# Kernel tuning notes

Hardware: AMD Instinct MI355X
Metric: run time of the kernel (lower is better)

The kernel has to match this reference:

```python
import jax, jax.numpy as jnp
import numpy as np

C = 64
HW = 21 * 21  # 441
NEIGHBOR_K = 3


def setup_inputs() -> dict:
    key = jax.random.key(0)
    k1, k2, k3, k4 = jax.random.split(key, 4)
    B1, B2 = 32, 25
    x1 = jax.random.normal(k1, (B1, C, 21, 21), dtype=jnp.float32)
    x2 = jax.random.normal(k2, (B2, C, 21, 21), dtype=jnp.float32)
    mask1 = jax.random.uniform(k3, (B1, 21, 21), dtype=jnp.float32)
    mask2 = jax.random.uniform(k4, (B2, 21, 21), dtype=jnp.float32)
    return {"x1": x1, "x2": x2, "mask1": mask1, "mask2": mask2}


def reference(x1, x2, mask1, mask2):
    B1 = x1.shape[0]
    B2 = x2.shape[0]
    q = x1.reshape(B1, C, HW)  # (B1, 64, 441) query descriptors
    s = x2.reshape(B2, C, HW)  # (B2, 64, 441) support descriptors
    # per-descriptor L2 norms over channel dim
    qn = jnp.linalg.norm(q, axis=1)  # (B1, 441)
    sn = jnp.linalg.norm(s, axis=1)  # (B2, 441)
    # cosine similarity between every query descriptor and every support descriptor
    inner = jnp.einsum('aci,bcj->abij', q, s)  # (B1, B2, 441, 441)
    sim = inner / (qn[:, None, :, None] * sn[None, :, None, :])
    # mask out invalid spatial positions on both sides
    sim = sim * mask1.reshape(B1, 1, HW, 1) * mask2.reshape(1, B2, 1, HW)
    # top-k nearest support descriptors per query descriptor, sum over all
    topk_vals, _ = jax.lax.top_k(sim, NEIGHBOR_K)  # (B1, B2, 441, k)
    return topk_vals.reshape(B1, B2, -1).sum(axis=2)  # (B1, B2)
```

## Files before the change

### kernel.cpp

```cpp
#include <hip/hip_runtime.h>
#include <math.h>

#define CCH 64
#define HW 441
#define HWP 448
#define NB2 25
#define PANEL (HWP * CCH)
#define TSTR 2048
#define NJT 14

typedef _Float16 half8 __attribute__((ext_vector_type(8)));
typedef __fp16 h2 __attribute__((ext_vector_type(2)));
typedef float f32x16 __attribute__((ext_vector_type(16)));

__global__ __launch_bounds__(64) void normalize_frag_kernel(
        const float* __restrict__ x1, const float* __restrict__ m1,
        const float* __restrict__ x2, const float* __restrict__ m2,
        _Float16* __restrict__ qh, _Float16* __restrict__ sh,
        float* __restrict__ out, int nout, int n1rows, int nrows) {
    int idx = blockIdx.x * blockDim.x + threadIdx.x;
    if (idx < nout) out[idx] = 0.f;
    if (idx >= nrows) return;
    const float* x; const float* mk; _Float16* outp; int rb;
    if (idx < n1rows) { x = x1; mk = m1; outp = qh; rb = idx; }
    else             { x = x2; mk = m2; outp = sh; rb = idx - n1rows; }
    int b = rb / HWP, i = rb - b * HWP;
    float vals[CCH];
    if (i < HW) {
        const float* xb = x + (size_t)b * CCH * HW + i;
        float ss = 0.f;
#pragma unroll
        for (int c = 0; c < CCH; ++c) { float v = xb[c * HW]; vals[c] = v; ss += v * v; }
        float scale = mk[b * HW + i] * rsqrtf(ss);
#pragma unroll
        for (int c = 0; c < CCH; ++c) vals[c] *= scale;
    } else {
#pragma unroll
        for (int c = 0; c < CCH; ++c) vals[c] = 0.f;
    }
    _Float16* pb = outp + (size_t)b * PANEL + (size_t)(i >> 5) * TSTR + (i & 31) * 8;
#pragma unroll
    for (int f = 0; f < 4; ++f) {
#pragma unroll
        for (int hh = 0; hh < 2; ++hh) {
            half8 h;
#pragma unroll
            for (int e = 0; e < 8; ++e) h[e] = (_Float16)vals[f * 16 + hh * 8 + e];
            *(half8*)(pb + f * 512 + hh * 256) = h;
        }
    }
}

static __device__ __forceinline__ h2 hmax2(h2 a, h2 b) {
    return __builtin_elementwise_max(a, b);
}
static __device__ __forceinline__ h2 hmin2(h2 a, h2 b) {
    return __builtin_elementwise_min(a, b);
}

#define PK_INSERT(v, p0, p1, p2)           \
    do {                                   \
        h2 _m = hmax2(p0, v);              \
        h2 _c = hmin2(p0, v);              \
        p0 = _m;                           \
        _m = hmax2(p1, _c);                \
        _c = hmin2(p1, _c);                \
        p1 = _m;                           \
        p2 = hmax2(p2, _c);                \
    } while (0)

#define MERGE3(t0, t1, t2, b0, b1, b2)            \
    do {                                          \
        float _m0 = fmaxf(t0, b0);                \
        float _n0 = fminf(t0, b0);                \
        float _m1 = fmaxf(t1, b1);                \
        float _t2 = fmaxf(t2, b2);                \
        t0 = _m0;                                 \
        t1 = fmaxf(_n0, _m1);                     \
        t2 = fmaxf(fminf(_n0, _m1), _t2);         \
    } while (0)

#define MFMA32(z, c, q) z = __builtin_amdgcn_mfma_f32_32x32x16_f16(c, q, z, 0, 0, 0)

__global__ __launch_bounds__(128, 5) void sim_topk_mfma(const _Float16* __restrict__ qh,
                                                        const _Float16* __restrict__ sh,
                                                        float* __restrict__ out) {
    int blk = blockIdx.x;
    int pair = blk / 7, g = blk - pair * 7;
    int a = pair / NB2, b = pair - a * NB2;
    int tid = threadIdx.x, wave = tid >> 6, lane = tid & 63;
    int hi = lane >> 5;
    const float NEG = -1e30f;
    const h2 NEGH = {(__fp16)-65504.f, (__fp16)-65504.f};

    const _Float16* qt = qh + (size_t)a * PANEL + (size_t)(g * 2 + wave) * TSTR + lane * 8;
    half8 qf0 = *(const half8*)(qt);
    half8 qf1 = *(const half8*)(qt + 512);
    half8 qf2 = *(const half8*)(qt + 1024);
    half8 qf3 = *(const half8*)(qt + 1536);

    const _Float16* sp = sh + (size_t)b * PANEL + lane * 8;
    half8 c0 = *(const half8*)(sp);
    half8 c1 = *(const half8*)(sp + 512);
    half8 c2 = *(const half8*)(sp + 1024);
    half8 c3 = *(const half8*)(sp + 1536);

    h2 p0 = NEGH, p1 = NEGH, p2 = NEGH;

    for (int jt = 0; jt < NJT - 1; ++jt) {
        const _Float16* np = sp + (size_t)(jt + 1) * TSTR;
        half8 n0 = *(const half8*)(np);
        half8 n1 = *(const half8*)(np + 512);
        half8 n2 = *(const half8*)(np + 1024);
        half8 n3 = *(const half8*)(np + 1536);

        f32x16 z = {0.f, 0.f, 0.f, 0.f, 0.f, 0.f, 0.f, 0.f,
                    0.f, 0.f, 0.f, 0.f, 0.f, 0.f, 0.f, 0.f};
        MFMA32(z, c0, qf0);
        MFMA32(z, c1, qf1);
        MFMA32(z, c2, qf2);
        MFMA32(z, c3, qf3);
#pragma unroll
        for (int r = 0; r < 8; ++r) {
            h2 c = __builtin_amdgcn_cvt_pkrtz(z[2 * r], z[2 * r + 1]);
            PK_INSERT(c, p0, p1, p2);
        }
        c0 = n0; c1 = n1; c2 = n2; c3 = n3;
    }

    {
        f32x16 z = {0.f, 0.f, 0.f, 0.f, 0.f, 0.f, 0.f, 0.f,
                    0.f, 0.f, 0.f, 0.f, 0.f, 0.f, 0.f, 0.f};
        MFMA32(z, c0, qf0);
        MFMA32(z, c1, qf1);
        MFMA32(z, c2, qf2);
        MFMA32(z, c3, qf3);
#pragma unroll
        for (int r = 0; r < 6; ++r) {
            h2 c = __builtin_amdgcn_cvt_pkrtz(z[2 * r], z[2 * r + 1]);
            PK_INSERT(c, p0, p1, p2);
        }
        float z12 = hi ? NEG : z[12];
        h2 c = __builtin_amdgcn_cvt_pkrtz(z12, NEG);
        PK_INSERT(c, p0, p1, p2);
    }

    float a0 = (float)p0[0], a1 = (float)p1[0], a2 = (float)p2[0];
    float b0 = (float)p0[1], b1 = (float)p1[1], b2 = (float)p2[1];
    MERGE3(a0, a1, a2, b0, b1, b2);
    b0 = __shfl_xor(a0, 32); b1 = __shfl_xor(a1, 32); b2 = __shfl_xor(a2, 32);
    MERGE3(a0, a1, a2, b0, b1, b2);
    float rsum = hi ? 0.f : (a0 + a1 + a2);
#pragma unroll
    for (int off = 32; off > 0; off >>= 1) rsum += __shfl_xor(rsum, off);
    if (lane == 0) atomicAdd(&out[pair], rsum);
}

extern "C" void kernel_launch(void* const* d_in, const int* in_sizes, int n_in,
                              void* d_out, int out_size, void* d_ws, size_t ws_size,
                              hipStream_t stream) {
    const float* x1 = (const float*)d_in[0];
    const float* x2 = (const float*)d_in[1];
    const float* m1 = (const float*)d_in[2];
    const float* m2 = (const float*)d_in[3];
    float* out = (float*)d_out;

    int B1 = in_sizes[0] / (CCH * HW);
    int B2 = in_sizes[1] / (CCH * HW);

    _Float16* qh = (_Float16*)d_ws;
    _Float16* sh = qh + (size_t)B1 * PANEL;

    int n1 = B1 * HWP, ntot = (B1 + B2) * HWP;
    normalize_frag_kernel<<<(ntot + 63) / 64, 64, 0, stream>>>(
        x1, m1, x2, m2, qh, sh, out, B1 * B2, n1, ntot);
    sim_topk_mfma<<<B1 * B2 * 7, 128, 0, stream>>>(qh, sh, out);
}
```

Measured before the change: 101.2 us.

## Have each wave process two query tiles, reusing support fragments

The similarity kernel now runs one wave per block, and that wave handles both 32-row query tiles that two waves previously split. Each support fragment loaded from memory feeds two MFMA chains, which halves support-panel loads per query tile and gives two independent accumulators for instruction-level parallelism. s_setprio is raised around the MFMA bursts so they get issue priority over other waves. Register pressure roughly doubles for accumulators and top-k state, launch bounds change to (64,4), and there are half as many waves in flight per block.

```diff
diff --git a/kernel.cpp b/kernel.cpp
--- a/kernel.cpp
+++ b/kernel.cpp
@@ -82,22 +82,28 @@
 
 #define MFMA32(z, c, q) z = __builtin_amdgcn_mfma_f32_32x32x16_f16(c, q, z, 0, 0, 0)
 
-__global__ __launch_bounds__(128, 5) void sim_topk_mfma(const _Float16* __restrict__ qh,
-                                                        const _Float16* __restrict__ sh,
-                                                        float* __restrict__ out) {
+__global__ __launch_bounds__(64, 4) void sim_topk_mfma(const _Float16* __restrict__ qh,
+                                                       const _Float16* __restrict__ sh,
+                                                       float* __restrict__ out) {
     int blk = blockIdx.x;
     int pair = blk / 7, g = blk - pair * 7;
     int a = pair / NB2, b = pair - a * NB2;
-    int tid = threadIdx.x, wave = tid >> 6, lane = tid & 63;
+    int lane = threadIdx.x;
     int hi = lane >> 5;
     const float NEG = -1e30f;
     const h2 NEGH = {(__fp16)-65504.f, (__fp16)-65504.f};
-
-    const _Float16* qt = qh + (size_t)a * PANEL + (size_t)(g * 2 + wave) * TSTR + lane * 8;
-    half8 qf0 = *(const half8*)(qt);
-    half8 qf1 = *(const half8*)(qt + 512);
-    half8 qf2 = *(const half8*)(qt + 1024);
-    half8 qf3 = *(const half8*)(qt + 1536);
+    const f32x16 FZ = {0.f, 0.f, 0.f, 0.f, 0.f, 0.f, 0.f, 0.f,
+                       0.f, 0.f, 0.f, 0.f, 0.f, 0.f, 0.f, 0.f};
+
+    const _Float16* qt = qh + (size_t)a * PANEL + (size_t)(g * 2) * TSTR + lane * 8;
+    half8 qa0 = *(const half8*)(qt);
+    half8 qa1 = *(const half8*)(qt + 512);
+    half8 qa2 = *(const half8*)(qt + 1024);
+    half8 qa3 = *(const half8*)(qt + 1536);
+    half8 qb0 = *(const half8*)(qt + 2048);
+    half8 qb1 = *(const half8*)(qt + 2560);
+    half8 qb2 = *(const half8*)(qt + 3072);
+    half8 qb3 = *(const half8*)(qt + 3584);
 
     const _Float16* sp = sh + (size_t)b * PANEL + lane * 8;
     half8 c0 = *(const half8*)(sp);
@@ -105,7 +111,8 @@
     half8 c2 = *(const half8*)(sp + 1024);
     half8 c3 = *(const half8*)(sp + 1536);
 
-    h2 p0 = NEGH, p1 = NEGH, p2 = NEGH;
+    h2 pa0 = NEGH, pa1 = NEGH, pa2 = NEGH;
+    h2 pb0 = NEGH, pb1 = NEGH, pb2 = NEGH;
 
     for (int jt = 0; jt < NJT - 1; ++jt) {
         const _Float16* np = sp + (size_t)(jt + 1) * TSTR;
@@ -114,43 +121,61 @@
         half8 n2 = *(const half8*)(np + 1024);
         half8 n3 = *(const half8*)(np + 1536);
 
-        f32x16 z = {0.f, 0.f, 0.f, 0.f, 0.f, 0.f, 0.f, 0.f,
-                    0.f, 0.f, 0.f, 0.f, 0.f, 0.f, 0.f, 0.f};
-        MFMA32(z, c0, qf0);
-        MFMA32(z, c1, qf1);
-        MFMA32(z, c2, qf2);
-        MFMA32(z, c3, qf3);
+        __builtin_amdgcn_s_setprio(1);
+        f32x16 z0 = FZ, z1 = FZ;
+        MFMA32(z0, c0, qa0); MFMA32(z1, c0, qb0);
+        MFMA32(z0, c1, qa1); MFMA32(z1, c1, qb1);
+        MFMA32(z0, c2, qa2); MFMA32(z1, c2, qb2);
+        MFMA32(z0, c3, qa3); MFMA32(z1, c3, qb3);
+        __builtin_amdgcn_s_setprio(0);
 #pragma unroll
         for (int r = 0; r < 8; ++r) {
-            h2 c = __builtin_amdgcn_cvt_pkrtz(z[2 * r], z[2 * r + 1]);
-            PK_INSERT(c, p0, p1, p2);
+            h2 ca = __builtin_amdgcn_cvt_pkrtz(z0[2 * r], z0[2 * r + 1]);
+            h2 cb = __builtin_amdgcn_cvt_pkrtz(z1[2 * r], z1[2 * r + 1]);
+            PK_INSERT(ca, pa0, pa1, pa2);
+            PK_INSERT(cb, pb0, pb1, pb2);
         }
         c0 = n0; c1 = n1; c2 = n2; c3 = n3;
     }
 
     {
-        f32x16 z = {0.f, 0.f, 0.f, 0.f, 0.f, 0.f, 0.f, 0.f,
-                    0.f, 0.f, 0.f, 0.f, 0.f, 0.f, 0.f, 0.f};
-        MFMA32(z, c0, qf0);
-        MFMA32(z, c1, qf1);
-        MFMA32(z, c2, qf2);
-        MFMA32(z, c3, qf3);
+        __builtin_amdgcn_s_setprio(1);
+        f32x16 z0 = FZ, z1 = FZ;
+        MFMA32(z0, c0, qa0); MFMA32(z1, c0, qb0);
+        MFMA32(z0, c1, qa1); MFMA32(z1, c1, qb1);
+        MFMA32(z0, c2, qa2); MFMA32(z1, c2, qb2);
+        MFMA32(z0, c3, qa3); MFMA32(z1, c3, qb3);
+        __builtin_amdgcn_s_setprio(0);
 #pragma unroll
         for (int r = 0; r < 6; ++r) {
-            h2 c = __builtin_amdgcn_cvt_pkrtz(z[2 * r], z[2 * r + 1]);
-            PK_INSERT(c, p0, p1, p2);
+            h2 ca = __builtin_amdgcn_cvt_pkrtz(z0[2 * r], z0[2 * r + 1]);
+            h2 cb = __builtin_amdgcn_cvt_pkrtz(z1[2 * r], z1[2 * r + 1]);
+            PK_INSERT(ca, pa0, pa1, pa2);
+            PK_INSERT(cb, pb0, pb1, pb2);
         }
-        float z12 = hi ? NEG : z[12];
-        h2 c = __builtin_amdgcn_cvt_pkrtz(z12, NEG);
-        PK_INSERT(c, p0, p1, p2);
-    }
-
-    float a0 = (float)p0[0], a1 = (float)p1[0], a2 = (float)p2[0];
-    float b0 = (float)p0[1], b1 = (float)p1[1], b2 = (float)p2[1];
+        float za = hi ? NEG : z0[12];
+        float zb = hi ? NEG : z1[12];
+        h2 ca = __builtin_amdgcn_cvt_pkrtz(za, NEG);
+        h2 cb = __builtin_amdgcn_cvt_pkrtz(zb, NEG);
+        PK_INSERT(ca, pa0, pa1, pa2);
+        PK_INSERT(cb, pb0, pb1, pb2);
+    }
+
+    float a0 = (float)pa0[0], a1 = (float)pa1[0], a2 = (float)pa2[0];
+    float b0 = (float)pa0[1], b1 = (float)pa1[1], b2 = (float)pa2[1];
     MERGE3(a0, a1, a2, b0, b1, b2);
     b0 = __shfl_xor(a0, 32); b1 = __shfl_xor(a1, 32); b2 = __shfl_xor(a2, 32);
     MERGE3(a0, a1, a2, b0, b1, b2);
-    float rsum = hi ? 0.f : (a0 + a1 + a2);
+    float suma = a0 + a1 + a2;
+
+    a0 = (float)pb0[0]; a1 = (float)pb1[0]; a2 = (float)pb2[0];
+    b0 = (float)pb0[1]; b1 = (float)pb1[1]; b2 = (float)pb2[1];
+    MERGE3(a0, a1, a2, b0, b1, b2);
+    b0 = __shfl_xor(a0, 32); b1 = __shfl_xor(a1, 32); b2 = __shfl_xor(a2, 32);
+    MERGE3(a0, a1, a2, b0, b1, b2);
+    float sumb = a0 + a1 + a2;
+
+    float rsum = hi ? 0.f : (suma + sumb);
 #pragma unroll
     for (int off = 32; off > 0; off >>= 1) rsum += __shfl_xor(rsum, off);
     if (lane == 0) atomicAdd(&out[pair], rsum);
@@ -174,5 +199,5 @@
     int n1 = B1 * HWP, ntot = (B1 + B2) * HWP;
     normalize_frag_kernel<<<(ntot + 63) / 64, 64, 0, stream>>>(
         x1, m1, x2, m2, qh, sh, out, B1 * B2, n1, ntot);
-    sim_topk_mfma<<<B1 * B2 * 7, 128, 0, stream>>>(qh, sh, out);
-}
+    sim_topk_mfma<<<B1 * B2 * 7, 64, 0, stream>>>(qh, sh, out);
+}
```

Result: faster. 97.43 us (-3.7%).

## Process seven query tiles per wave to reuse support fragments across MFMAs

Applied to the files above, without the earlier changes.

Each single-wave block now holds seven query tiles in registers and streams the support panel once, issuing paired MFMAs against the same support fragments. This cuts redundant support loads (previously re-read by seven blocks per pair) and gives two independent MFMA chains to hide latency, and s_setprio is raised around the compute. In exchange register pressure rises sharply (28 query fragments plus 21 top-k registers) and the grid shrinks from 5600 two-wave blocks to 1600 one-wave blocks, which may reduce occupancy and latency hiding.

```diff
diff --git a/kernel.cpp b/kernel.cpp
--- a/kernel.cpp
+++ b/kernel.cpp
@@ -82,22 +82,96 @@
 
 #define MFMA32(z, c, q) z = __builtin_amdgcn_mfma_f32_32x32x16_f16(c, q, z, 0, 0, 0)
 
-__global__ __launch_bounds__(128, 5) void sim_topk_mfma(const _Float16* __restrict__ qh,
-                                                        const _Float16* __restrict__ sh,
-                                                        float* __restrict__ out) {
+#define DO_PAIR(ta, tb)                                                     \
+    do {                                                                    \
+        f32x16 z0 = FZ, z1 = FZ;                                            \
+        MFMA32(z0, c0, qf##ta##0); MFMA32(z1, c0, qf##tb##0);               \
+        MFMA32(z0, c1, qf##ta##1); MFMA32(z1, c1, qf##tb##1);               \
+        MFMA32(z0, c2, qf##ta##2); MFMA32(z1, c2, qf##tb##2);               \
+        MFMA32(z0, c3, qf##ta##3); MFMA32(z1, c3, qf##tb##3);               \
+        _Pragma("unroll")                                                   \
+        for (int r = 0; r < 8; ++r) {                                       \
+            h2 ca = __builtin_amdgcn_cvt_pkrtz(z0[2 * r], z0[2 * r + 1]);   \
+            h2 cb = __builtin_amdgcn_cvt_pkrtz(z1[2 * r], z1[2 * r + 1]);   \
+            PK_INSERT(ca, p0[ta], p1[ta], p2[ta]);                          \
+            PK_INSERT(cb, p0[tb], p1[tb], p2[tb]);                          \
+        }                                                                   \
+    } while (0)
+
+#define DO_SINGLE(ta)                                                       \
+    do {                                                                    \
+        f32x16 z0 = FZ;                                                     \
+        MFMA32(z0, c0, qf##ta##0);                                          \
+        MFMA32(z0, c1, qf##ta##1);                                          \
+        MFMA32(z0, c2, qf##ta##2);                                          \
+        MFMA32(z0, c3, qf##ta##3);                                          \
+        _Pragma("unroll")                                                   \
+        for (int r = 0; r < 8; ++r) {                                       \
+            h2 ca = __builtin_amdgcn_cvt_pkrtz(z0[2 * r], z0[2 * r + 1]);   \
+            PK_INSERT(ca, p0[ta], p1[ta], p2[ta]);                          \
+        }                                                                   \
+    } while (0)
+
+#define DO_PAIR_M(ta, tb)                                                   \
+    do {                                                                    \
+        f32x16 z0 = FZ, z1 = FZ;                                            \
+        MFMA32(z0, c0, qf##ta##0); MFMA32(z1, c0, qf##tb##0);               \
+        MFMA32(z0, c1, qf##ta##1); MFMA32(z1, c1, qf##tb##1);               \
+        MFMA32(z0, c2, qf##ta##2); MFMA32(z1, c2, qf##tb##2);               \
+        MFMA32(z0, c3, qf##ta##3); MFMA32(z1, c3, qf##tb##3);               \
+        _Pragma("unroll")                                                   \
+        for (int r = 0; r < 6; ++r) {                                       \
+            h2 ca = __builtin_amdgcn_cvt_pkrtz(z0[2 * r], z0[2 * r + 1]);   \
+            h2 cb = __builtin_amdgcn_cvt_pkrtz(z1[2 * r], z1[2 * r + 1]);   \
+            PK_INSERT(ca, p0[ta], p1[ta], p2[ta]);                          \
+            PK_INSERT(cb, p0[tb], p1[tb], p2[tb]);                          \
+        }                                                                   \
+        float za = hi ? NEG : z0[12];                                       \
+        float zb = hi ? NEG : z1[12];                                       \
+        h2 ca = __builtin_amdgcn_cvt_pkrtz(za, NEG);                        \
+        h2 cb = __builtin_amdgcn_cvt_pkrtz(zb, NEG);                        \
+        PK_INSERT(ca, p0[ta], p1[ta], p2[ta]);                              \
+        PK_INSERT(cb, p0[tb], p1[tb], p2[tb]);                              \
+    } while (0)
+
+#define DO_SINGLE_M(ta)                                                     \
+    do {                                                                    \
+        f32x16 z0 = FZ;                                                     \
+        MFMA32(z0, c0, qf##ta##0);                                          \
+        MFMA32(z0, c1, qf##ta##1);                                          \
+        MFMA32(z0, c2, qf##ta##2);                                          \
+        MFMA32(z0, c3, qf##ta##3);                                          \
+        _Pragma("unroll")                                                   \
+        for (int r = 0; r < 6; ++r) {                                       \
+            h2 ca = __builtin_amdgcn_cvt_pkrtz(z0[2 * r], z0[2 * r + 1]);   \
+            PK_INSERT(ca, p0[ta], p1[ta], p2[ta]);                          \
+        }                                                                   \
+        float za = hi ? NEG : z0[12];                                       \
+        h2 ca = __builtin_amdgcn_cvt_pkrtz(za, NEG);                        \
+        PK_INSERT(ca, p0[ta], p1[ta], p2[ta]);                              \
+    } while (0)
+
+#define LOAD_Q(t)                                                           \
+    half8 qf##t##0 = *(const half8*)(qt + (t) * 2048);                      \
+    half8 qf##t##1 = *(const half8*)(qt + (t) * 2048 + 512);                \
+    half8 qf##t##2 = *(const half8*)(qt + (t) * 2048 + 1024);               \
+    half8 qf##t##3 = *(const half8*)(qt + (t) * 2048 + 1536);
+
+__global__ __launch_bounds__(64, 2) void sim_topk_mfma(const _Float16* __restrict__ qh,
+                                                       const _Float16* __restrict__ sh,
+                                                       float* __restrict__ out) {
     int blk = blockIdx.x;
-    int pair = blk / 7, g = blk - pair * 7;
+    int pair = blk >> 1, g = blk & 1;
     int a = pair / NB2, b = pair - a * NB2;
-    int tid = threadIdx.x, wave = tid >> 6, lane = tid & 63;
+    int lane = threadIdx.x;
     int hi = lane >> 5;
     const float NEG = -1e30f;
     const h2 NEGH = {(__fp16)-65504.f, (__fp16)-65504.f};
-
-    const _Float16* qt = qh + (size_t)a * PANEL + (size_t)(g * 2 + wave) * TSTR + lane * 8;
-    half8 qf0 = *(const half8*)(qt);
-    half8 qf1 = *(const half8*)(qt + 512);
-    half8 qf2 = *(const half8*)(qt + 1024);
-    half8 qf3 = *(const half8*)(qt + 1536);
+    const f32x16 FZ = {0.f, 0.f, 0.f, 0.f, 0.f, 0.f, 0.f, 0.f,
+                       0.f, 0.f, 0.f, 0.f, 0.f, 0.f, 0.f, 0.f};
+
+    const _Float16* qt = qh + (size_t)a * PANEL + (size_t)(g * 7) * TSTR + lane * 8;
+    LOAD_Q(0) LOAD_Q(1) LOAD_Q(2) LOAD_Q(3) LOAD_Q(4) LOAD_Q(5) LOAD_Q(6)
 
     const _Float16* sp = sh + (size_t)b * PANEL + lane * 8;
     half8 c0 = *(const half8*)(sp);
@@ -105,7 +179,9 @@
     half8 c2 = *(const half8*)(sp + 1024);
     half8 c3 = *(const half8*)(sp + 1536);
 
-    h2 p0 = NEGH, p1 = NEGH, p2 = NEGH;
+    h2 p0[7], p1[7], p2[7];
+#pragma unroll
+    for (int t = 0; t < 7; ++t) { p0[t] = NEGH; p1[t] = NEGH; p2[t] = NEGH; }
 
     for (int jt = 0; jt < NJT - 1; ++jt) {
         const _Float16* np = sp + (size_t)(jt + 1) * TSTR;
@@ -114,43 +190,35 @@
         half8 n2 = *(const half8*)(np + 1024);
         half8 n3 = *(const half8*)(np + 1536);
 
-        f32x16 z = {0.f, 0.f, 0.f, 0.f, 0.f, 0.f, 0.f, 0.f,
-                    0.f, 0.f, 0.f, 0.f, 0.f, 0.f, 0.f, 0.f};
-        MFMA32(z, c0, qf0);
-        MFMA32(z, c1, qf1);
-        MFMA32(z, c2, qf2);
-        MFMA32(z, c3, qf3);
-#pragma unroll
-        for (int r = 0; r < 8; ++r) {
-            h2 c = __builtin_amdgcn_cvt_pkrtz(z[2 * r], z[2 * r + 1]);
-            PK_INSERT(c, p0, p1, p2);
-        }
+        __builtin_amdgcn_s_setprio(1);
+        DO_PAIR(0, 1);
+        DO_PAIR(2, 3);
+        DO_PAIR(4, 5);
+        DO_SINGLE(6);
+        __builtin_amdgcn_s_setprio(0);
         c0 = n0; c1 = n1; c2 = n2; c3 = n3;
     }
 
     {
-        f32x16 z = {0.f, 0.f, 0.f, 0.f, 0.f, 0.f, 0.f, 0.f,
-                    0.f, 0.f, 0.f, 0.f, 0.f, 0.f, 0.f, 0.f};
-        MFMA32(z, c0, qf0);
-        MFMA32(z, c1, qf1);
-        MFMA32(z, c2, qf2);
-        MFMA32(z, c3, qf3);
-#pragma unroll
-        for (int r = 0; r < 6; ++r) {
-            h2 c = __builtin_amdgcn_cvt_pkrtz(z[2 * r], z[2 * r + 1]);
-            PK_INSERT(c, p0, p1, p2);
-        }
-        float z12 = hi ? NEG : z[12];
-        h2 c = __builtin_amdgcn_cvt_pkrtz(z12, NEG);
-        PK_INSERT(c, p0, p1, p2);
-    }
-
-    float a0 = (float)p0[0], a1 = (float)p1[0], a2 = (float)p2[0];
-    float b0 = (float)p0[1], b1 = (float)p1[1], b2 = (float)p2[1];
-    MERGE3(a0, a1, a2, b0, b1, b2);
-    b0 = __shfl_xor(a0, 32); b1 = __shfl_xor(a1, 32); b2 = __shfl_xor(a2, 32);
-    MERGE3(a0, a1, a2, b0, b1, b2);
-    float rsum = hi ? 0.f : (a0 + a1 + a2);
+        __builtin_amdgcn_s_setprio(1);
+        DO_PAIR_M(0, 1);
+        DO_PAIR_M(2, 3);
+        DO_PAIR_M(4, 5);
+        DO_SINGLE_M(6);
+        __builtin_amdgcn_s_setprio(0);
+    }
+
+    float rsum = 0.f;
+#pragma unroll
+    for (int t = 0; t < 7; ++t) {
+        float a0 = (float)p0[t][0], a1 = (float)p1[t][0], a2 = (float)p2[t][0];
+        float b0 = (float)p0[t][1], b1 = (float)p1[t][1], b2 = (float)p2[t][1];
+        MERGE3(a0, a1, a2, b0, b1, b2);
+        b0 = __shfl_xor(a0, 32); b1 = __shfl_xor(a1, 32); b2 = __shfl_xor(a2, 32);
+        MERGE3(a0, a1, a2, b0, b1, b2);
+        rsum += a0 + a1 + a2;
+    }
+    rsum = hi ? 0.f : rsum;
 #pragma unroll
     for (int off = 32; off > 0; off >>= 1) rsum += __shfl_xor(rsum, off);
     if (lane == 0) atomicAdd(&out[pair], rsum);
@@ -174,5 +242,5 @@
     int n1 = B1 * HWP, ntot = (B1 + B2) * HWP;
     normalize_frag_kernel<<<(ntot + 63) / 64, 64, 0, stream>>>(
         x1, m1, x2, m2, qh, sh, out, B1 * B2, n1, ntot);
-    sim_topk_mfma<<<B1 * B2 * 7, 128, 0, stream>>>(qh, sh, out);
-}
+    sim_topk_mfma<<<B1 * B2 * 2, 64, 0, stream>>>(qh, sh, out);
+}
```

After: 96.99 us. 4.1% less time.
